# Kernel optimization log

Measured on AMD Instinct MI355X. Metric: run time of the kernel, lower is better.

The kernel has to match this reference:

```python
import jax, jax.numpy as jnp
import numpy as np

INPUT_SIZE = 512
HIDDEN_SIZE = 256
B, S = 8, 2048


def setup_inputs() -> dict:
    key = jax.random.key(0)
    ks = jax.random.split(key, 9)
    d = INPUT_SIZE
    q = jax.random.normal(ks[0], (B, S, 2 * HIDDEN_SIZE), dtype=jnp.float32)
    k = jax.random.normal(ks[1], (B, S, d), dtype=jnp.float32)
    v = jax.random.normal(ks[2], (B, S, d), dtype=jnp.float32)
    # Params: module uses nn.init.normal_ (std=1); keep normal but scale for stability.
    Wq = jax.random.normal(ks[3], (2 * HIDDEN_SIZE, d), dtype=jnp.float32) * 0.02
    bq = jax.random.normal(ks[4], (d,), dtype=jnp.float32) * 0.02
    Wk = jax.random.normal(ks[5], (d, d), dtype=jnp.float32) * 0.02
    bk = jax.random.normal(ks[6], (d,), dtype=jnp.float32) * 0.02
    Wv = jax.random.normal(ks[7], (d, d), dtype=jnp.float32) * 0.02
    bv = jax.random.normal(ks[8], (d,), dtype=jnp.float32) * 0.02
    return {"q": q, "k": k, "v": v, "Wq": Wq, "bq": bq, "Wk": Wk, "bk": bk, "Wv": Wv, "bv": bv}


def reference(q, k, v, Wq, bq, Wk, bk, Wv, bv):
    d = Wq.shape[-1]
    qp = jnp.einsum('bsh,hd->bsd', q, Wq) + bq  # [B,S,d]
    kp = jnp.einsum('bse,ed->bsd', k, Wk) + bk
    vp = jnp.einsum('bse,ed->bsd', v, Wv) + bv
    scale = 1.0 / jnp.sqrt(jnp.float32(d))
    scores = jnp.einsum('bqd,bkd->bqk', qp, kp) * scale  # [B,S,S]
    attn = jax.nn.softmax(scores, axis=-1)
    return jnp.einsum('bqk,bkd->bqd', attn, vp)
```

## Files before the change

### kernel.cpp

```cpp
#include <hip/hip_runtime.h>
#include <hip/hip_bf16.h>
#include <stdint.h>


typedef __attribute__((ext_vector_type(8))) short short8;
typedef __attribute__((ext_vector_type(4))) float floatx4;

__device__ __forceinline__ unsigned short f2bf(float f) {
    union { float f; uint32_t u; } v; v.f = f;
    uint32_t u = v.u;
    return (unsigned short)((u + 0x7FFF + ((u >> 16) & 1)) >> 16);
}

#define ASYNC16(g, l)                                                          \
    __builtin_amdgcn_global_load_lds(                                          \
        (const __attribute__((address_space(1))) unsigned int*)(g),            \
        (__attribute__((address_space(3))) unsigned int*)(l), 16, 0, 0)

__global__ void wt_kernel(const float* __restrict__ Wq, const float* __restrict__ Wk,
                          const float* __restrict__ Wv, unsigned short* __restrict__ WT) {
    __shared__ float t[64][65];
    const int z = blockIdx.z;
    const float* W = (z == 0) ? Wq : ((z == 1) ? Wk : Wv);
    const int n0 = blockIdx.x * 64, k0 = blockIdx.y * 64;
    const int tx = threadIdx.x & 63, ty = threadIdx.x >> 6;
#pragma unroll
    for (int i = ty; i < 64; i += 4) t[i][tx] = W[(size_t)(k0 + i) * 512 + n0 + tx];
    __syncthreads();
#pragma unroll
    for (int i = ty; i < 64; i += 4)
        WT[(size_t)z * 262144 + (size_t)(n0 + i) * 512 + k0 + tx] = f2bf(t[tx][i]);
}

__global__ __launch_bounds__(256, 4) void proj_kernel(
    const float* __restrict__ q, const float* __restrict__ k, const float* __restrict__ v,
    const float* __restrict__ bq, const float* __restrict__ bk, const float* __restrict__ bv,
    const unsigned short* __restrict__ WT,
    unsigned short* __restrict__ qp, unsigned short* __restrict__ kp,
    unsigned short* __restrict__ vpT)
{
    __shared__ __align__(16) unsigned short At[2][64][32];
    __shared__ __align__(16) unsigned short Bt[2][256][32];

    const int z = blockIdx.z;
    const int tid = threadIdx.x;
    const int lane = tid & 63;
    const int wave = tid >> 6;
    const int col = lane & 15;
    const int quad = lane >> 4;

    const float* A = (z == 0) ? q : ((z == 1) ? k : v);
    const float* bias = (z == 0) ? bq : ((z == 1) ? bk : bv);
    const unsigned short* W = WT + (size_t)z * 262144;

    const int m0 = blockIdx.x * 64;
    const int n0b = blockIdx.y * 256;

    floatx4 acc[4][4];
#pragma unroll
    for (int mf = 0; mf < 4; ++mf)
#pragma unroll
        for (int nf = 0; nf < 4; ++nf) acc[mf][nf] = floatx4{0.f, 0.f, 0.f, 0.f};

    auto stageB = [&](int nb, int kc) {
#pragma unroll
        for (int j = 0; j < 4; ++j) {
            const int rr = (wave * 4 + j) * 16 + (lane >> 2);
            const unsigned short* g =
                W + (size_t)(n0b + rr) * 512 + kc * 32 + (((lane & 3) ^ ((rr >> 1) & 3)) << 3);
            ASYNC16(g, &Bt[nb][(wave * 4 + j) * 16][0]);
        }
    };

    float4 fA0, fA1;
    const int arow = tid >> 2;
    auto loadA = [&](int kc) {
        const float* ap = A + (size_t)(m0 + arow) * 512 + kc * 32 + (tid & 3) * 8;
        fA0 = *(const float4*)ap;
        fA1 = *(const float4*)(ap + 4);
    };
    auto writeA = [&](int nb) {
        short8 t;
        t[0] = f2bf(fA0.x); t[1] = f2bf(fA0.y); t[2] = f2bf(fA0.z); t[3] = f2bf(fA0.w);
        t[4] = f2bf(fA1.x); t[5] = f2bf(fA1.y); t[6] = f2bf(fA1.z); t[7] = f2bf(fA1.w);
        *(short8*)&At[nb][arow][(((tid & 3) ^ ((arow >> 1) & 3)) << 3)] = t;
    };

    stageB(0, 0);
    loadA(0);
    writeA(0);
    for (int kc = 0; kc < 16; ++kc) {
        const int cur = kc & 1;
        __syncthreads();
        if (kc < 15) { stageB(cur ^ 1, kc + 1); loadA(kc + 1); }

        const int rsw = (quad ^ ((col >> 1) & 3)) << 3;
        short8 a[4], bfr[4];
#pragma unroll
        for (int mf = 0; mf < 4; ++mf)
            a[mf] = *(const short8*)&At[cur][mf * 16 + col][rsw];
#pragma unroll
        for (int nf = 0; nf < 4; ++nf)
            bfr[nf] = *(const short8*)&Bt[cur][wave * 64 + nf * 16 + col][rsw];
#pragma unroll
        for (int mf = 0; mf < 4; ++mf)
#pragma unroll
            for (int nf = 0; nf < 4; ++nf)
                acc[mf][nf] = __builtin_amdgcn_mfma_f32_16x16x32_bf16(a[mf], bfr[nf], acc[mf][nf], 0, 0, 0);

        if (kc < 15) writeA(cur ^ 1);
    }

    const float scale = (z == 0) ? 0.04419417382415922f : 1.0f;
#pragma unroll
    for (int mf = 0; mf < 4; ++mf) {
#pragma unroll
        for (int nf = 0; nf < 4; ++nf) {
            const int n = n0b + wave * 64 + nf * 16 + col;
            const float bn2 = bias[n];
            floatx4 c = acc[mf][nf];
            if (z < 2) {
                unsigned short* outp = (z == 0) ? qp : kp;
#pragma unroll
                for (int r = 0; r < 4; ++r) {
                    int row = m0 + mf * 16 + quad * 4 + r;
                    outp[(size_t)row * 512 + n] = f2bf((c[r] + bn2) * scale);
                }
            } else {
                int row = m0 + mf * 16 + quad * 4;
                int bb = row >> 11;
                int s = row & 2047;
                ushort4 pk;
                pk.x = f2bf(c[0] + bn2); pk.y = f2bf(c[1] + bn2);
                pk.z = f2bf(c[2] + bn2); pk.w = f2bf(c[3] + bn2);
                *(ushort4*)(vpT + (((size_t)bb * 64 + (s >> 5)) * 512 + n) * 32 + (s & 31)) = pk;
            }
        }
    }
}

__global__ __launch_bounds__(512, 2) void attn_kernel(
    const unsigned short* __restrict__ qp, const unsigned short* __restrict__ kp,
    const unsigned short* __restrict__ vpT,
    float* __restrict__ Opart, float* __restrict__ lws)
{
    __shared__ __align__(16) unsigned short Kt[2][32][512];
    __shared__ __align__(16) unsigned short Vt[2][512][32];
    __shared__ __align__(16) unsigned short Pbuf[8][16][40];

    const int lane = threadIdx.x & 63;
    const int wave = threadIdx.x >> 6;
    const int col = lane & 15;
    const int quad = lane >> 4;
    const int b = blockIdx.x & 7;
    const int qt = (blockIdx.x >> 3) & 15;
    const int ksp = blockIdx.x >> 7;
    const int q0 = qt * 128 + wave * 16;
    const size_t rowbase = (size_t)b * 2048 + q0;

    const unsigned short* kpb = kp + (size_t)b * 2048 * 512;
    const unsigned short* vpb = vpT + ((size_t)b << 20);

    short8 aq[16];
#pragma unroll
    for (int kk = 0; kk < 16; ++kk)
        aq[kk] = *(const short8*)(qp + (rowbase + col) * 512 + kk * 32 + quad * 8);

    floatx4 o[32];
#pragma unroll
    for (int i = 0; i < 32; ++i) o[i] = floatx4{0.f, 0.f, 0.f, 0.f};
    float plsum[4] = {0.f, 0.f, 0.f, 0.f};

    auto stage = [&](int nb, int keyblk) {
#pragma unroll
        for (int j = 0; j < 4; ++j) {
            const int r = wave * 4 + j;
            const unsigned short* g =
                kpb + ((size_t)(keyblk * 32 + r) << 9) + ((lane ^ (r & 7)) << 3);
            ASYNC16(g, &Kt[nb][r][0]);
        }
        const unsigned short* vtile = vpb + ((size_t)keyblk << 14);
#pragma unroll
        for (int jj = 0; jj < 4; ++jj) {
            const int j2 = wave * 4 + jj;
            const int d = j2 * 16 + (lane >> 2);
            const unsigned short* g =
                vtile + ((size_t)d << 5) + (((lane & 3) ^ ((d >> 1) & 3)) << 3);
            ASYNC16(g, &Vt[nb][j2 * 16][0]);
        }
    };

    stage(0, ksp * 32);
    for (int kb = 0; kb < 32; ++kb) {
        const int cur = kb & 1;
        __syncthreads();
        if (kb < 31) stage(cur ^ 1, ksp * 32 + kb + 1);

        floatx4 s0 = floatx4{0.f, 0.f, 0.f, 0.f};
        floatx4 s1 = floatx4{0.f, 0.f, 0.f, 0.f};
        __builtin_amdgcn_s_setprio(1);
#pragma unroll
        for (int kk = 0; kk < 16; ++kk) {
            const int c = (kk << 2) + quad;
            short8 b0 = *(const short8*)&Kt[cur][col][(c ^ (col & 7)) << 3];
            short8 b1 = *(const short8*)&Kt[cur][16 + col][(c ^ (col & 7)) << 3];
            s0 = __builtin_amdgcn_mfma_f32_16x16x32_bf16(aq[kk], b0, s0, 0, 0, 0);
            s1 = __builtin_amdgcn_mfma_f32_16x16x32_bf16(aq[kk], b1, s1, 0, 0, 0);
        }
        __builtin_amdgcn_s_setprio(0);

#pragma unroll
        for (int r = 0; r < 4; ++r) {
            const float p0 = __expf(s0[r]);
            const float p1 = __expf(s1[r]);
            plsum[r] += p0 + p1;
            Pbuf[wave][quad * 4 + r][col]      = f2bf(p0);
            Pbuf[wave][quad * 4 + r][16 + col] = f2bf(p1);
        }
        const short8 aP = *(const short8*)&Pbuf[wave][col][quad * 8];

        __builtin_amdgcn_s_setprio(1);
#pragma unroll
        for (int nf = 0; nf < 32; ++nf) {
            const int d = nf * 16 + col;
            short8 bvf = *(const short8*)&Vt[cur][d][(quad ^ ((d >> 1) & 3)) << 3];
            o[nf] = __builtin_amdgcn_mfma_f32_16x16x32_bf16(aP, bvf, o[nf], 0, 0, 0);
        }
        __builtin_amdgcn_s_setprio(0);
    }

    float l[4];
#pragma unroll
    for (int r = 0; r < 4; ++r) {
        float acc_s = plsum[r];
#pragma unroll
        for (int off = 1; off <= 8; off <<= 1)
            acc_s += __shfl_xor(acc_s, off, 64);
        l[r] = acc_s;
    }
    const size_t g16 = rowbase >> 4;
    float* ob = Opart + (size_t)ksp * 8388608 + g16 * 8192 + quad * 64 + col;
#pragma unroll
    for (int nf = 0; nf < 32; ++nf) {
#pragma unroll
        for (int r = 0; r < 4; ++r) {
            ob[nf * 256 + r * 16] = o[nf][r];
        }
    }
    if (col == 0) {
        float* lp = lws + ksp * 16384 + (int)rowbase;
#pragma unroll
        for (int r = 0; r < 4; ++r) lp[quad * 4 + r] = l[r];
    }
}

__global__ __launch_bounds__(256) void norm_kernel(float* __restrict__ out,
                                                   const float* __restrict__ Opart,
                                                   const float* __restrict__ lws)
{
    const size_t gid = (size_t)blockIdx.x * 256 + threadIdx.x;
    const int row = (int)(gid >> 7);
    const int d = ((int)gid & 127) * 4;
    const float rl = 1.0f / (lws[row] + lws[16384 + row]);
    const size_t src = ((size_t)(row >> 4)) * 8192 + (d >> 4) * 256 +
                       ((row & 15) >> 2) * 64 + (row & 3) * 16 + (d & 15);
    float4 a = *(const float4*)(Opart + src);
    float4 c = *(const float4*)(Opart + 8388608 + src);
    float4 r;
    r.x = (a.x + c.x) * rl; r.y = (a.y + c.y) * rl;
    r.z = (a.z + c.z) * rl; r.w = (a.w + c.w) * rl;
    *(float4*)(out + (size_t)row * 512 + d) = r;
}

extern "C" void kernel_launch(void* const* d_in, const int* in_sizes, int n_in,
                              void* d_out, int out_size, void* d_ws, size_t ws_size,
                              hipStream_t stream) {
    const float* q  = (const float*)d_in[0];
    const float* k  = (const float*)d_in[1];
    const float* v  = (const float*)d_in[2];
    const float* Wq = (const float*)d_in[3];
    const float* bq = (const float*)d_in[4];
    const float* Wk = (const float*)d_in[5];
    const float* bk = (const float*)d_in[6];
    const float* Wv = (const float*)d_in[7];
    const float* bv = (const float*)d_in[8];
    float* out = (float*)d_out;

    unsigned short* WT  = (unsigned short*)d_ws;
    unsigned short* qp  = WT + (size_t)3 * 262144;
    unsigned short* kp  = qp + (size_t)16384 * 512;
    unsigned short* vpT = kp + (size_t)16384 * 512;
    float* Opart = (float*)(vpT + (size_t)16384 * 512);
    float* lws   = Opart + (size_t)2 * 16384 * 512;

    wt_kernel<<<dim3(8, 8, 3), 256, 0, stream>>>(Wq, Wk, Wv, WT);
    proj_kernel<<<dim3(256, 2, 3), 256, 0, stream>>>(q, k, v, bq, bk, bv, WT, qp, kp, vpT);
    attn_kernel<<<256, 512, 0, stream>>>(qp, kp, vpT, Opart, lws);
    norm_kernel<<<8192, 256, 0, stream>>>(out, Opart, lws);
}
```

Before: 316.5 us.

## Give each attention wave two 16-row query tiles to reuse K/V LDS fragments

The attention block shrinks from 8 waves to 4, and each wave now handles 32 query rows as two 16-row groups. Every K fragment and V fragment read from LDS feeds two MFMAs instead of one, which halves LDS read traffic per unit of MFMA work. The cost is twice the accumulator and Q registers per wave (o grows to 64 floatx4) and fewer waves to hide latency. Launch bounds drop to 256 threads and one block per SIMD setting, which risks lower occupancy or register spills.

```diff
diff --git a/kernel.cpp b/kernel.cpp
--- a/kernel.cpp
+++ b/kernel.cpp
@@ -139,14 +139,14 @@
     }
 }
 
-__global__ __launch_bounds__(512, 2) void attn_kernel(
+__global__ __launch_bounds__(256, 1) void attn_kernel(
     const unsigned short* __restrict__ qp, const unsigned short* __restrict__ kp,
     const unsigned short* __restrict__ vpT,
     float* __restrict__ Opart, float* __restrict__ lws)
 {
     __shared__ __align__(16) unsigned short Kt[2][32][512];
     __shared__ __align__(16) unsigned short Vt[2][512][32];
-    __shared__ __align__(16) unsigned short Pbuf[8][16][40];
+    __shared__ __align__(16) unsigned short Pbuf[4][32][40];
 
     const int lane = threadIdx.x & 63;
     const int wave = threadIdx.x >> 6;
@@ -155,34 +155,38 @@
     const int b = blockIdx.x & 7;
     const int qt = (blockIdx.x >> 3) & 15;
     const int ksp = blockIdx.x >> 7;
-    const int q0 = qt * 128 + wave * 16;
+    const int q0 = qt * 128 + wave * 32;
     const size_t rowbase = (size_t)b * 2048 + q0;
 
     const unsigned short* kpb = kp + (size_t)b * 2048 * 512;
     const unsigned short* vpb = vpT + ((size_t)b << 20);
 
-    short8 aq[16];
-#pragma unroll
-    for (int kk = 0; kk < 16; ++kk)
-        aq[kk] = *(const short8*)(qp + (rowbase + col) * 512 + kk * 32 + quad * 8);
-
-    floatx4 o[32];
-#pragma unroll
-    for (int i = 0; i < 32; ++i) o[i] = floatx4{0.f, 0.f, 0.f, 0.f};
-    float plsum[4] = {0.f, 0.f, 0.f, 0.f};
+    short8 aq[2][16];
+#pragma unroll
+    for (int g = 0; g < 2; ++g)
+#pragma unroll
+        for (int kk = 0; kk < 16; ++kk)
+            aq[g][kk] = *(const short8*)(qp + (rowbase + g * 16 + col) * 512 + kk * 32 + quad * 8);
+
+    floatx4 o[2][32];
+#pragma unroll
+    for (int g = 0; g < 2; ++g)
+#pragma unroll
+        for (int i = 0; i < 32; ++i) o[g][i] = floatx4{0.f, 0.f, 0.f, 0.f};
+    float plsum[2][4] = {{0.f, 0.f, 0.f, 0.f}, {0.f, 0.f, 0.f, 0.f}};
 
     auto stage = [&](int nb, int keyblk) {
 #pragma unroll
-        for (int j = 0; j < 4; ++j) {
-            const int r = wave * 4 + j;
+        for (int j = 0; j < 8; ++j) {
+            const int r = wave * 8 + j;
             const unsigned short* g =
                 kpb + ((size_t)(keyblk * 32 + r) << 9) + ((lane ^ (r & 7)) << 3);
             ASYNC16(g, &Kt[nb][r][0]);
         }
         const unsigned short* vtile = vpb + ((size_t)keyblk << 14);
 #pragma unroll
-        for (int jj = 0; jj < 4; ++jj) {
-            const int j2 = wave * 4 + jj;
+        for (int jj = 0; jj < 8; ++jj) {
+            const int j2 = wave * 8 + jj;
             const int d = j2 * 16 + (lane >> 2);
             const unsigned short* g =
                 vtile + ((size_t)d << 5) + (((lane & 3) ^ ((d >> 1) & 3)) << 3);
@@ -196,61 +200,75 @@
         __syncthreads();
         if (kb < 31) stage(cur ^ 1, ksp * 32 + kb + 1);
 
-        floatx4 s0 = floatx4{0.f, 0.f, 0.f, 0.f};
-        floatx4 s1 = floatx4{0.f, 0.f, 0.f, 0.f};
+        floatx4 s00 = floatx4{0.f, 0.f, 0.f, 0.f};
+        floatx4 s01 = floatx4{0.f, 0.f, 0.f, 0.f};
+        floatx4 s10 = floatx4{0.f, 0.f, 0.f, 0.f};
+        floatx4 s11 = floatx4{0.f, 0.f, 0.f, 0.f};
         __builtin_amdgcn_s_setprio(1);
 #pragma unroll
         for (int kk = 0; kk < 16; ++kk) {
             const int c = (kk << 2) + quad;
             short8 b0 = *(const short8*)&Kt[cur][col][(c ^ (col & 7)) << 3];
             short8 b1 = *(const short8*)&Kt[cur][16 + col][(c ^ (col & 7)) << 3];
-            s0 = __builtin_amdgcn_mfma_f32_16x16x32_bf16(aq[kk], b0, s0, 0, 0, 0);
-            s1 = __builtin_amdgcn_mfma_f32_16x16x32_bf16(aq[kk], b1, s1, 0, 0, 0);
+            s00 = __builtin_amdgcn_mfma_f32_16x16x32_bf16(aq[0][kk], b0, s00, 0, 0, 0);
+            s01 = __builtin_amdgcn_mfma_f32_16x16x32_bf16(aq[0][kk], b1, s01, 0, 0, 0);
+            s10 = __builtin_amdgcn_mfma_f32_16x16x32_bf16(aq[1][kk], b0, s10, 0, 0, 0);
+            s11 = __builtin_amdgcn_mfma_f32_16x16x32_bf16(aq[1][kk], b1, s11, 0, 0, 0);
         }
         __builtin_amdgcn_s_setprio(0);
 
 #pragma unroll
         for (int r = 0; r < 4; ++r) {
-            const float p0 = __expf(s0[r]);
-            const float p1 = __expf(s1[r]);
-            plsum[r] += p0 + p1;
-            Pbuf[wave][quad * 4 + r][col]      = f2bf(p0);
-            Pbuf[wave][quad * 4 + r][16 + col] = f2bf(p1);
-        }
-        const short8 aP = *(const short8*)&Pbuf[wave][col][quad * 8];
+            const float p00 = __expf(s00[r]);
+            const float p01 = __expf(s01[r]);
+            plsum[0][r] += p00 + p01;
+            Pbuf[wave][quad * 4 + r][col]      = f2bf(p00);
+            Pbuf[wave][quad * 4 + r][16 + col] = f2bf(p01);
+            const float p10 = __expf(s10[r]);
+            const float p11 = __expf(s11[r]);
+            plsum[1][r] += p10 + p11;
+            Pbuf[wave][16 + quad * 4 + r][col]      = f2bf(p10);
+            Pbuf[wave][16 + quad * 4 + r][16 + col] = f2bf(p11);
+        }
+        const short8 aP0 = *(const short8*)&Pbuf[wave][col][quad * 8];
+        const short8 aP1 = *(const short8*)&Pbuf[wave][16 + col][quad * 8];
 
         __builtin_amdgcn_s_setprio(1);
 #pragma unroll
         for (int nf = 0; nf < 32; ++nf) {
             const int d = nf * 16 + col;
             short8 bvf = *(const short8*)&Vt[cur][d][(quad ^ ((d >> 1) & 3)) << 3];
-            o[nf] = __builtin_amdgcn_mfma_f32_16x16x32_bf16(aP, bvf, o[nf], 0, 0, 0);
+            o[0][nf] = __builtin_amdgcn_mfma_f32_16x16x32_bf16(aP0, bvf, o[0][nf], 0, 0, 0);
+            o[1][nf] = __builtin_amdgcn_mfma_f32_16x16x32_bf16(aP1, bvf, o[1][nf], 0, 0, 0);
         }
         __builtin_amdgcn_s_setprio(0);
     }
 
-    float l[4];
-#pragma unroll
-    for (int r = 0; r < 4; ++r) {
-        float acc_s = plsum[r];
-#pragma unroll
-        for (int off = 1; off <= 8; off <<= 1)
-            acc_s += __shfl_xor(acc_s, off, 64);
-        l[r] = acc_s;
-    }
-    const size_t g16 = rowbase >> 4;
-    float* ob = Opart + (size_t)ksp * 8388608 + g16 * 8192 + quad * 64 + col;
-#pragma unroll
-    for (int nf = 0; nf < 32; ++nf) {
+#pragma unroll
+    for (int g = 0; g < 2; ++g) {
+        float l[4];
 #pragma unroll
         for (int r = 0; r < 4; ++r) {
-            ob[nf * 256 + r * 16] = o[nf][r];
-        }
-    }
-    if (col == 0) {
-        float* lp = lws + ksp * 16384 + (int)rowbase;
-#pragma unroll
-        for (int r = 0; r < 4; ++r) lp[quad * 4 + r] = l[r];
+            float acc_s = plsum[g][r];
+#pragma unroll
+            for (int off = 1; off <= 8; off <<= 1)
+                acc_s += __shfl_xor(acc_s, off, 64);
+            l[r] = acc_s;
+        }
+        const size_t g16 = (rowbase >> 4) + g;
+        float* ob = Opart + (size_t)ksp * 8388608 + g16 * 8192 + quad * 64 + col;
+#pragma unroll
+        for (int nf = 0; nf < 32; ++nf) {
+#pragma unroll
+            for (int r = 0; r < 4; ++r) {
+                ob[nf * 256 + r * 16] = o[g][nf][r];
+            }
+        }
+        if (col == 0) {
+            float* lp = lws + ksp * 16384 + (int)rowbase + g * 16;
+#pragma unroll
+            for (int r = 0; r < 4; ++r) lp[quad * 4 + r] = l[r];
+        }
     }
 }
 
@@ -295,6 +313,6 @@
 
     wt_kernel<<<dim3(8, 8, 3), 256, 0, stream>>>(Wq, Wk, Wv, WT);
     proj_kernel<<<dim3(256, 2, 3), 256, 0, stream>>>(q, k, v, bq, bk, bv, WT, qp, kp, vpT);
-    attn_kernel<<<256, 512, 0, stream>>>(qp, kp, vpT, Opart, lws);
+    attn_kernel<<<256, 256, 0, stream>>>(qp, kp, vpT, Opart, lws);
     norm_kernel<<<8192, 256, 0, stream>>>(out, Opart, lws);
 }
```

Measured after the change: 315.2 us. Within noise of the previous version (-0.4%).
